# Optimization experiments

Hardware: AMD Instinct MI355X
Metric: run time of the kernel (lower is better)

The kernel has to match this reference:

```python
import jax, jax.numpy as jnp
import numpy as np

B, L, D, H = 4, 1024, 1024, 16
DH = D // H


def setup_inputs() -> dict:
    key = jax.random.key(0)
    ks = jax.random.split(key, 10)
    x_embed = jax.random.normal(ks[0], (B, L, D), dtype=jnp.float32)
    bemb = jax.random.normal(ks[1], (B, L), dtype=jnp.float32)
    s = 0.02
    Wq_w = jax.random.normal(ks[2], (D, D), dtype=jnp.float32) * s
    Wk_w = jax.random.normal(ks[3], (D, D), dtype=jnp.float32) * s
    Wv_w = jax.random.normal(ks[4], (D, D), dtype=jnp.float32) * s
    Wo_w = jax.random.normal(ks[5], (D, D), dtype=jnp.float32) * s
    Wq_b = jnp.zeros((D,), jnp.float32)
    Wk_b = jnp.zeros((D,), jnp.float32)
    Wv_b = jnp.zeros((D,), jnp.float32)
    Wo_b = jnp.zeros((D,), jnp.float32)
    return dict(x_embed=x_embed, bemb=bemb, Wq_w=Wq_w, Wq_b=Wq_b,
                Wk_w=Wk_w, Wk_b=Wk_b, Wv_w=Wv_w, Wv_b=Wv_b,
                Wo_w=Wo_w, Wo_b=Wo_b)


def reference(x_embed, bemb, Wq_w, Wq_b, Wk_w, Wk_b, Wv_w, Wv_b, Wo_w, Wo_b):
    # present[b, l] = token l of batch b participates in attention
    present = bemb > 0  # [B, L]

    def proj(w, b):
        # torch Linear: y = x W^T + b; split heads -> [B, H, L, DH]
        y = jnp.einsum('bld,ed->ble', x_embed, w) + b
        return y.reshape(B, L, H, DH).transpose(0, 2, 1, 3)

    Q = proj(Wq_w, Wq_b)
    K = proj(Wk_w, Wk_b)
    V = proj(Wv_w, Wv_b)

    scores = jnp.einsum('bhqd,bhkd->bhqk', Q, K) / jnp.sqrt(jnp.float32(DH))
    # pre-softmax column mask: absent keys -> -inf
    scores = jnp.where(present[:, None, None, :], scores, -jnp.inf)
    A = jax.nn.softmax(scores, axis=-1)  # [B, H, L, L]
    # post-softmax row mask: subtract 1 on absent query rows, then relu
    row_absent = (~present).astype(A.dtype)[:, None, :, None]  # [B,1,L,1]
    A = jnp.maximum(A - row_absent, 0.0)

    out = jnp.einsum('bhqk,bhkd->bhqd', A, V)
    out = out.transpose(0, 2, 1, 3).reshape(B, L, D)
    out = jnp.einsum('bld,ed->ble', out, Wo_w) + Wo_b
    return out, A
```

## Files before the change

### kernel.cpp

```cpp
#include <hip/hip_runtime.h>
#include <math.h>

#define BB 4
#define LL 1024
#define DD 1024
#define HH 16
#define MROWS 4096

typedef __attribute__((ext_vector_type(8))) short short8;
typedef __attribute__((ext_vector_type(4))) float f32x4;
typedef __attribute__((ext_vector_type(4))) unsigned short us4;

__device__ inline unsigned short f2bf(float f) {
    unsigned int u = __builtin_bit_cast(unsigned int, f);
    u += 0x7fffu + ((u >> 16) & 1u);
    return (unsigned short)(u >> 16);
}

__global__ __launch_bounds__(256) void cvt_bf16(const float* __restrict__ src,
                                                unsigned short* __restrict__ dst,
                                                int n4) {
    int i = blockIdx.x * 256 + threadIdx.x;
    if (i < n4) {
        float4 v = ((const float4*)src)[i];
        us4 p = { f2bf(v.x), f2bf(v.y), f2bf(v.z), f2bf(v.w) };
        ((us4*)dst)[i] = p;
    }
}

template<int OUT_MODE>
__global__ __launch_bounds__(256) void gemm128(const unsigned short* __restrict__ X,
                                               const unsigned short* __restrict__ W,
                                               const float* __restrict__ bias,
                                               void* __restrict__ Cv) {
    __shared__ unsigned short Xs[128][72];
    __shared__ unsigned short Ws[128][72];
    const int t = threadIdx.x;
    const int lane = t & 63, quad = lane >> 4, lm = lane & 15;
    const int wave = t >> 6;
    const int mo = (wave & 1) * 64, no = (wave >> 1) * 64;
    const int row0 = blockIdx.x * 128, col0 = blockIdx.y * 128;

    f32x4 acc[4][4] = {};

    for (int kc = 0; kc < 1024; kc += 64) {
        #pragma unroll
        for (int i = 0; i < 4; ++i) {
            int id = t + 256 * i; int r = id >> 3, sg = id & 7;
            *(short8*)&Xs[r][sg * 8] =
                *(const short8*)&X[(size_t)(row0 + r) * 1024 + kc + sg * 8];
            *(short8*)&Ws[r][sg * 8] =
                *(const short8*)&W[(size_t)(col0 + r) * 1024 + kc + sg * 8];
        }
        __syncthreads();
        #pragma unroll
        for (int s = 0; s < 2; ++s) {
            short8 af[4], bf[4];
            #pragma unroll
            for (int mi = 0; mi < 4; ++mi)
                af[mi] = *(const short8*)&Xs[mo + mi * 16 + lm][s * 32 + quad * 8];
            #pragma unroll
            for (int nj = 0; nj < 4; ++nj)
                bf[nj] = *(const short8*)&Ws[no + nj * 16 + lm][s * 32 + quad * 8];
            #pragma unroll
            for (int mi = 0; mi < 4; ++mi)
                #pragma unroll
                for (int nj = 0; nj < 4; ++nj)
                    acc[mi][nj] = __builtin_amdgcn_mfma_f32_16x16x32_bf16(
                        af[mi], bf[nj], acc[mi][nj], 0, 0, 0);
        }
        __syncthreads();
    }

    #pragma unroll
    for (int mi = 0; mi < 4; ++mi) {
        #pragma unroll
        for (int nj = 0; nj < 4; ++nj) {
            int gr0 = row0 + mo + mi * 16 + quad * 4;
            int gc  = col0 + no + nj * 16 + lm;
            float bv = bias[gc];
            #pragma unroll
            for (int r = 0; r < 4; ++r) {
                float val = acc[mi][nj][r] + bv;
                int gr = gr0 + r;
                if (OUT_MODE == 0) {
                    ((float*)Cv)[(size_t)gr * 1024 + gc] = val;
                } else if (OUT_MODE == 1) {
                    ((unsigned short*)Cv)[(size_t)gr * 1024 + gc] = f2bf(val);
                } else {
                    int bb = gr >> 10, l = gr & 1023;
                    int hh = gc >> 6,  dd = gc & 63;
                    ((unsigned short*)Cv)[(((size_t)bb * 16 + hh) * 64 + dd) * 1024 + l] = f2bf(val);
                }
            }
        }
    }
}

__global__ __launch_bounds__(512) void attn_fused(const unsigned short* __restrict__ Qw,
                                                  const unsigned short* __restrict__ Kw,
                                                  const unsigned short* __restrict__ Vt,
                                                  const float* __restrict__ bemb,
                                                  float* __restrict__ Aout,
                                                  unsigned short* __restrict__ attn) {
    __shared__ unsigned short Ks[128][72];
    __shared__ unsigned short Vs[64][136];
    __shared__ unsigned short Ps[8][16][132];
    __shared__ float maskadd[1024];
    const int t = threadIdx.x;
    const int lane = t & 63, quad = lane >> 4, lm = lane & 15;
    const int w = t >> 6;
    const int q0 = blockIdx.x * 128;
    const int bh = blockIdx.y;
    const int b = bh >> 4, h = bh & 15;
    const int qrow_frag = q0 + w * 16 + lm;
    const int qrow_acc0 = q0 + w * 16 + quad * 4;

    for (int i = t; i < 1024; i += 512)
        maskadd[i] = (bemb[b * 1024 + i] > 0.f) ? 0.f : -1e30f;

    short8 afq[2];
    #pragma unroll
    for (int s = 0; s < 2; ++s)
        afq[s] = *(const short8*)&Qw[(size_t)(b * 1024 + qrow_frag) * 1024 +
                                     h * 64 + s * 32 + quad * 8];

    float mrun[4], lrun[4];
    #pragma unroll
    for (int r = 0; r < 4; ++r) { mrun[r] = -INFINITY; lrun[r] = 0.f; }

    __syncthreads();

    for (int c = 0; c < 8; ++c) {
        __syncthreads();
        #pragma unroll
        for (int i = 0; i < 2; ++i) {
            int id = t + 512 * i; int r = id >> 3, sg = id & 7;
            *(short8*)&Ks[r][sg * 8] =
                *(const short8*)&Kw[(size_t)(b * 1024 + c * 128 + r) * 1024 +
                                    h * 64 + sg * 8];
        }
        __syncthreads();

        f32x4 acc[8] = {};
        #pragma unroll
        for (int s = 0; s < 2; ++s)
            #pragma unroll
            for (int nj = 0; nj < 8; ++nj) {
                short8 bfk = *(const short8*)&Ks[nj * 16 + lm][s * 32 + quad * 8];
                acc[nj] = __builtin_amdgcn_mfma_f32_16x16x32_bf16(afq[s], bfk, acc[nj], 0, 0, 0);
            }

        float cmax[4] = { -INFINITY, -INFINITY, -INFINITY, -INFINITY };
        #pragma unroll
        for (int nj = 0; nj < 8; ++nj) {
            float ma = maskadd[c * 128 + nj * 16 + lm];
            #pragma unroll
            for (int r = 0; r < 4; ++r) {
                float sv = acc[nj][r] * 0.125f + ma;
                acc[nj][r] = sv;
                cmax[r] = fmaxf(cmax[r], sv);
            }
        }
        #pragma unroll
        for (int r = 0; r < 4; ++r) {
            #pragma unroll
            for (int off = 8; off >= 1; off >>= 1)
                cmax[r] = fmaxf(cmax[r], __shfl_xor(cmax[r], off, 64));
            float mnew = fmaxf(mrun[r], cmax[r]);
            float csum = 0.f;
            #pragma unroll
            for (int nj = 0; nj < 8; ++nj)
                csum += __expf(acc[nj][r] - mnew);
            #pragma unroll
            for (int off = 8; off >= 1; off >>= 1)
                csum += __shfl_xor(csum, off, 64);
            lrun[r] = lrun[r] * __expf(mrun[r] - mnew) + csum;
            mrun[r] = mnew;
        }
    }

    float fnorm[4];
    #pragma unroll
    for (int r = 0; r < 4; ++r) {
        bool qp = bemb[b * 1024 + qrow_acc0 + r] > 0.f;
        fnorm[r] = (qp && lrun[r] > 0.f) ? (1.f / lrun[r]) : 0.f;
    }

    f32x4 oacc[4] = {};
    for (int c = 0; c < 8; ++c) {
        __syncthreads();
        #pragma unroll
        for (int i = 0; i < 2; ++i) {
            int id = t + 512 * i;
            { int r = id >> 3, sg = id & 7;
              *(short8*)&Ks[r][sg * 8] =
                  *(const short8*)&Kw[(size_t)(b * 1024 + c * 128 + r) * 1024 +
                                      h * 64 + sg * 8]; }
            { int r = id >> 4, sg = id & 15;
              *(short8*)&Vs[r][sg * 8] =
                  *(const short8*)&Vt[((size_t)bh * 64 + r) * 1024 + c * 128 + sg * 8]; }
        }
        __syncthreads();

        f32x4 acc[8] = {};
        #pragma unroll
        for (int s = 0; s < 2; ++s)
            #pragma unroll
            for (int nj = 0; nj < 8; ++nj) {
                short8 bfk = *(const short8*)&Ks[nj * 16 + lm][s * 32 + quad * 8];
                acc[nj] = __builtin_amdgcn_mfma_f32_16x16x32_bf16(afq[s], bfk, acc[nj], 0, 0, 0);
            }

        #pragma unroll
        for (int nj = 0; nj < 8; ++nj) {
            float ma = maskadd[c * 128 + nj * 16 + lm];
            #pragma unroll
            for (int r = 0; r < 4; ++r) {
                float sv = acc[nj][r] * 0.125f + ma;
                float p  = __expf(sv - mrun[r]);
                float a  = p * fnorm[r];
                Aout[((size_t)bh * 1024 + qrow_acc0 + r) * 1024 + c * 128 + nj * 16 + lm] = a;
                Ps[w][quad * 4 + r][nj * 16 + lm] = f2bf(a);
            }
        }

        #pragma unroll
        for (int ks = 0; ks < 4; ++ks) {
            short8 afp = *(const short8*)&Ps[w][lm][ks * 32 + quad * 8];
            #pragma unroll
            for (int nd = 0; nd < 4; ++nd) {
                short8 bfv = *(const short8*)&Vs[nd * 16 + lm][ks * 32 + quad * 8];
                oacc[nd] = __builtin_amdgcn_mfma_f32_16x16x32_bf16(afp, bfv, oacc[nd], 0, 0, 0);
            }
        }
    }

    #pragma unroll
    for (int nd = 0; nd < 4; ++nd)
        #pragma unroll
        for (int r = 0; r < 4; ++r)
            attn[(size_t)(b * 1024 + qrow_acc0 + r) * 1024 + h * 64 + nd * 16 + lm] =
                f2bf(oacc[nd][r]);
}

extern "C" void kernel_launch(void* const* d_in, const int* in_sizes, int n_in,
                              void* d_out, int out_size, void* d_ws, size_t ws_size,
                              hipStream_t stream) {
    const float* x    = (const float*)d_in[0];
    const float* bemb = (const float*)d_in[1];
    const float* Wq   = (const float*)d_in[2];
    const float* Wq_b = (const float*)d_in[3];
    const float* Wk   = (const float*)d_in[4];
    const float* Wk_b = (const float*)d_in[5];
    const float* Wv   = (const float*)d_in[6];
    const float* Wv_b = (const float*)d_in[7];
    const float* Wo   = (const float*)d_in[8];
    const float* Wo_b = (const float*)d_in[9];

    float* out  = (float*)d_out;
    float* Aout = out + (size_t)BB * LL * DD;

    unsigned short* x_bf  = (unsigned short*)d_ws;
    unsigned short* Wq_bf = x_bf  + (size_t)MROWS * DD;
    unsigned short* Wk_bf = Wq_bf + (size_t)DD * DD;
    unsigned short* Wv_bf = Wk_bf + (size_t)DD * DD;
    unsigned short* Wo_bf = Wv_bf + (size_t)DD * DD;
    unsigned short* Qw    = Wo_bf + (size_t)DD * DD;
    unsigned short* Kw    = Qw + (size_t)MROWS * DD;
    unsigned short* Vt    = Kw + (size_t)MROWS * DD;
    unsigned short* Aw    = x_bf;

    dim3 blk(256);
    const int n4x = MROWS * DD / 4;
    const int n4w = DD * DD / 4;
    cvt_bf16<<<dim3(n4x / 256), blk, 0, stream>>>(x,  x_bf,  n4x);
    cvt_bf16<<<dim3(n4w / 256), blk, 0, stream>>>(Wq, Wq_bf, n4w);
    cvt_bf16<<<dim3(n4w / 256), blk, 0, stream>>>(Wk, Wk_bf, n4w);
    cvt_bf16<<<dim3(n4w / 256), blk, 0, stream>>>(Wv, Wv_bf, n4w);
    cvt_bf16<<<dim3(n4w / 256), blk, 0, stream>>>(Wo, Wo_bf, n4w);

    dim3 pgrid(MROWS / 128, DD / 128);
    gemm128<1><<<pgrid, blk, 0, stream>>>(x_bf, Wq_bf, Wq_b, Qw);
    gemm128<1><<<pgrid, blk, 0, stream>>>(x_bf, Wk_bf, Wk_b, Kw);
    gemm128<2><<<pgrid, blk, 0, stream>>>(x_bf, Wv_bf, Wv_b, Vt);

    attn_fused<<<dim3(LL / 128, BB * HH), dim3(512), 0, stream>>>(
        Qw, Kw, Vt, bemb, Aout, Aw);

    gemm128<0><<<pgrid, blk, 0, stream>>>(Aw, Wo_bf, Wo_b, out);
}
```

Measured before the change: 468.5 us.

## Use direct global-to-LDS loads with XOR swizzle and merge launches

Replaces the register-staged global→LDS copies in the GEMM and attention kernels with global_load_lds 16-byte direct loads. The LDS tiles lose their padding and use an XOR swizzle to avoid bank conflicts. The five conversion kernels are merged into one launch, and the three QKV GEMMs into one launch using a z grid dimension. This is meant to cut VGPR staging, LDS bank conflicts and launch overhead. The cost is a runtime out_mode branch in the GEMM epilogue and dependence on the swizzle matching the direct-load address mapping.

```diff
diff --git a/kernel.cpp b/kernel.cpp
--- a/kernel.cpp
+++ b/kernel.cpp
@@ -17,40 +17,63 @@
     return (unsigned short)(u >> 16);
 }
 
-__global__ __launch_bounds__(256) void cvt_bf16(const float* __restrict__ src,
-                                                unsigned short* __restrict__ dst,
-                                                int n4) {
+__device__ inline void gl2lds16(const void* g, void* l) {
+    __builtin_amdgcn_global_load_lds(
+        (const __attribute__((address_space(1))) void*)g,
+        (__attribute__((address_space(3))) void*)l, 16, 0, 0);
+}
+
+__global__ __launch_bounds__(256) void cvt_all(const float* __restrict__ x,
+                                               const float* __restrict__ wq,
+                                               const float* __restrict__ wk,
+                                               const float* __restrict__ wv,
+                                               const float* __restrict__ wo,
+                                               unsigned short* __restrict__ xb,
+                                               unsigned short* __restrict__ wqb,
+                                               unsigned short* __restrict__ wkb,
+                                               unsigned short* __restrict__ wvb,
+                                               unsigned short* __restrict__ wob) {
     int i = blockIdx.x * 256 + threadIdx.x;
-    if (i < n4) {
-        float4 v = ((const float4*)src)[i];
-        us4 p = { f2bf(v.x), f2bf(v.y), f2bf(v.z), f2bf(v.w) };
-        ((us4*)dst)[i] = p;
-    }
-}
-
-template<int OUT_MODE>
-__global__ __launch_bounds__(256) void gemm128(const unsigned short* __restrict__ X,
-                                               const unsigned short* __restrict__ W,
-                                               const float* __restrict__ bias,
-                                               void* __restrict__ Cv) {
-    __shared__ unsigned short Xs[128][72];
-    __shared__ unsigned short Ws[128][72];
+    const float* src; unsigned short* dst; int k;
+    if (i < 1048576) { src = x; dst = xb; k = i; }
+    else {
+        int j = i - 1048576; int w = j >> 18; k = j & 262143;
+        src = (w == 0) ? wq : (w == 1) ? wk : (w == 2) ? wv : wo;
+        dst = (w == 0) ? wqb : (w == 1) ? wkb : (w == 2) ? wvb : wob;
+    }
+    float4 v = ((const float4*)src)[k];
+    us4 p = { f2bf(v.x), f2bf(v.y), f2bf(v.z), f2bf(v.w) };
+    ((us4*)dst)[k] = p;
+}
+
+__device__ __forceinline__ void gemm_core(const unsigned short* __restrict__ X,
+                                          const unsigned short* __restrict__ W,
+                                          const float* __restrict__ bias,
+                                          void* __restrict__ Cv, int out_mode) {
+    __shared__ unsigned short Xs[128][64];
+    __shared__ unsigned short Ws[128][64];
     const int t = threadIdx.x;
     const int lane = t & 63, quad = lane >> 4, lm = lane & 15;
     const int wave = t >> 6;
     const int mo = (wave & 1) * 64, no = (wave >> 1) * 64;
     const int row0 = blockIdx.x * 128, col0 = blockIdx.y * 128;
+    const int sw = lm & 7;
+
+    const int r_in = lane >> 3;
+    const int sg = (lane & 7) ^ r_in;
+    const int lrow = wave * 32 + r_in;
+    const unsigned short* xp = X + (size_t)(row0 + lrow) * 1024 + sg * 8;
+    const unsigned short* wp = W + (size_t)(col0 + lrow) * 1024 + sg * 8;
+    unsigned short* ldsX = &Xs[wave * 32][0];
+    unsigned short* ldsW = &Ws[wave * 32][0];
 
     f32x4 acc[4][4] = {};
 
     for (int kc = 0; kc < 1024; kc += 64) {
         #pragma unroll
-        for (int i = 0; i < 4; ++i) {
-            int id = t + 256 * i; int r = id >> 3, sg = id & 7;
-            *(short8*)&Xs[r][sg * 8] =
-                *(const short8*)&X[(size_t)(row0 + r) * 1024 + kc + sg * 8];
-            *(short8*)&Ws[r][sg * 8] =
-                *(const short8*)&W[(size_t)(col0 + r) * 1024 + kc + sg * 8];
+        for (int j = 0; j < 4; ++j) {
+            gl2lds16(xp + (size_t)j * 8192 + kc, ldsX + j * 512);
+            gl2lds16(wp + (size_t)j * 8192 + kc, ldsW + j * 512);
         }
         __syncthreads();
         #pragma unroll
@@ -58,10 +81,10 @@
             short8 af[4], bf[4];
             #pragma unroll
             for (int mi = 0; mi < 4; ++mi)
-                af[mi] = *(const short8*)&Xs[mo + mi * 16 + lm][s * 32 + quad * 8];
+                af[mi] = *(const short8*)&Xs[mo + mi * 16 + lm][((s * 4 + quad) ^ sw) * 8];
             #pragma unroll
             for (int nj = 0; nj < 4; ++nj)
-                bf[nj] = *(const short8*)&Ws[no + nj * 16 + lm][s * 32 + quad * 8];
+                bf[nj] = *(const short8*)&Ws[no + nj * 16 + lm][((s * 4 + quad) ^ sw) * 8];
             #pragma unroll
             for (int mi = 0; mi < 4; ++mi)
                 #pragma unroll
@@ -83,9 +106,9 @@
             for (int r = 0; r < 4; ++r) {
                 float val = acc[mi][nj][r] + bv;
                 int gr = gr0 + r;
-                if (OUT_MODE == 0) {
+                if (out_mode == 0) {
                     ((float*)Cv)[(size_t)gr * 1024 + gc] = val;
-                } else if (OUT_MODE == 1) {
+                } else if (out_mode == 1) {
                     ((unsigned short*)Cv)[(size_t)gr * 1024 + gc] = f2bf(val);
                 } else {
                     int bb = gr >> 10, l = gr & 1023;
@@ -97,14 +120,38 @@
     }
 }
 
+__global__ __launch_bounds__(256) void qkv_proj(const unsigned short* __restrict__ xb,
+                                                const unsigned short* __restrict__ wq,
+                                                const unsigned short* __restrict__ wk,
+                                                const unsigned short* __restrict__ wv,
+                                                const float* __restrict__ bq,
+                                                const float* __restrict__ bk,
+                                                const float* __restrict__ bv,
+                                                unsigned short* __restrict__ Qw,
+                                                unsigned short* __restrict__ Kw,
+                                                unsigned short* __restrict__ Vt) {
+    const int z = blockIdx.z;
+    const unsigned short* W = (z == 0) ? wq : (z == 1) ? wk : wv;
+    const float* b = (z == 0) ? bq : (z == 1) ? bk : bv;
+    void* C = (z == 0) ? (void*)Qw : (z == 1) ? (void*)Kw : (void*)Vt;
+    gemm_core(xb, W, b, C, (z == 2) ? 2 : 1);
+}
+
+__global__ __launch_bounds__(256) void out_proj(const unsigned short* __restrict__ Aw,
+                                                const unsigned short* __restrict__ wo,
+                                                const float* __restrict__ bo,
+                                                float* __restrict__ out) {
+    gemm_core(Aw, wo, bo, out, 0);
+}
+
 __global__ __launch_bounds__(512) void attn_fused(const unsigned short* __restrict__ Qw,
                                                   const unsigned short* __restrict__ Kw,
                                                   const unsigned short* __restrict__ Vt,
                                                   const float* __restrict__ bemb,
                                                   float* __restrict__ Aout,
                                                   unsigned short* __restrict__ attn) {
-    __shared__ unsigned short Ks[128][72];
-    __shared__ unsigned short Vs[64][136];
+    __shared__ unsigned short Ks[128][64];
+    __shared__ unsigned short Vs[64][128];
     __shared__ unsigned short Ps[8][16][132];
     __shared__ float maskadd[1024];
     const int t = threadIdx.x;
@@ -115,6 +162,16 @@
     const int b = bh >> 4, h = bh & 15;
     const int qrow_frag = q0 + w * 16 + lm;
     const int qrow_acc0 = q0 + w * 16 + quad * 4;
+    const int swk = lm & 7;
+
+    const int kr_in = lane >> 3;
+    const int ksg = (lane & 7) ^ kr_in;
+    const unsigned short* kp = Kw + (size_t)(b * 1024 + w * 16 + kr_in) * 1024 + h * 64 + ksg * 8;
+    unsigned short* ldsK = &Ks[w * 16][0];
+    const int vr_in = lane >> 4, vcg = lane & 15;
+    const int vrow = w * 8 + vr_in;
+    const unsigned short* vpbase = Vt + (size_t)bh * 64 * 1024;
+    unsigned short* ldsV = &Vs[w * 8][0];
 
     for (int i = t; i < 1024; i += 512)
         maskadd[i] = (bemb[b * 1024 + i] > 0.f) ? 0.f : -1e30f;
@@ -132,14 +189,9 @@
     __syncthreads();
 
     for (int c = 0; c < 8; ++c) {
-        __syncthreads();
-        #pragma unroll
-        for (int i = 0; i < 2; ++i) {
-            int id = t + 512 * i; int r = id >> 3, sg = id & 7;
-            *(short8*)&Ks[r][sg * 8] =
-                *(const short8*)&Kw[(size_t)(b * 1024 + c * 128 + r) * 1024 +
-                                    h * 64 + sg * 8];
-        }
+        #pragma unroll
+        for (int j = 0; j < 2; ++j)
+            gl2lds16(kp + (size_t)(c * 128 + j * 8) * 1024, ldsK + j * 512);
         __syncthreads();
 
         f32x4 acc[8] = {};
@@ -147,7 +199,7 @@
         for (int s = 0; s < 2; ++s)
             #pragma unroll
             for (int nj = 0; nj < 8; ++nj) {
-                short8 bfk = *(const short8*)&Ks[nj * 16 + lm][s * 32 + quad * 8];
+                short8 bfk = *(const short8*)&Ks[nj * 16 + lm][((s * 4 + quad) ^ swk) * 8];
                 acc[nj] = __builtin_amdgcn_mfma_f32_16x16x32_bf16(afq[s], bfk, acc[nj], 0, 0, 0);
             }
 
@@ -178,6 +230,7 @@
             lrun[r] = lrun[r] * __expf(mrun[r] - mnew) + csum;
             mrun[r] = mnew;
         }
+        __syncthreads();
     }
 
     float fnorm[4];
@@ -189,17 +242,12 @@
 
     f32x4 oacc[4] = {};
     for (int c = 0; c < 8; ++c) {
-        __syncthreads();
-        #pragma unroll
-        for (int i = 0; i < 2; ++i) {
-            int id = t + 512 * i;
-            { int r = id >> 3, sg = id & 7;
-              *(short8*)&Ks[r][sg * 8] =
-                  *(const short8*)&Kw[(size_t)(b * 1024 + c * 128 + r) * 1024 +
-                                      h * 64 + sg * 8]; }
-            { int r = id >> 4, sg = id & 15;
-              *(short8*)&Vs[r][sg * 8] =
-                  *(const short8*)&Vt[((size_t)bh * 64 + r) * 1024 + c * 128 + sg * 8]; }
+        #pragma unroll
+        for (int j = 0; j < 2; ++j) {
+            gl2lds16(kp + (size_t)(c * 128 + j * 8) * 1024, ldsK + j * 512);
+            int rl = vrow + j * 4;
+            int vsg = vcg ^ (rl & 15);
+            gl2lds16(vpbase + (size_t)rl * 1024 + c * 128 + vsg * 8, ldsV + j * 512);
         }
         __syncthreads();
 
@@ -208,7 +256,7 @@
         for (int s = 0; s < 2; ++s)
             #pragma unroll
             for (int nj = 0; nj < 8; ++nj) {
-                short8 bfk = *(const short8*)&Ks[nj * 16 + lm][s * 32 + quad * 8];
+                short8 bfk = *(const short8*)&Ks[nj * 16 + lm][((s * 4 + quad) ^ swk) * 8];
                 acc[nj] = __builtin_amdgcn_mfma_f32_16x16x32_bf16(afq[s], bfk, acc[nj], 0, 0, 0);
             }
 
@@ -230,10 +278,11 @@
             short8 afp = *(const short8*)&Ps[w][lm][ks * 32 + quad * 8];
             #pragma unroll
             for (int nd = 0; nd < 4; ++nd) {
-                short8 bfv = *(const short8*)&Vs[nd * 16 + lm][ks * 32 + quad * 8];
+                short8 bfv = *(const short8*)&Vs[nd * 16 + lm][((ks * 4 + quad) ^ lm) * 8];
                 oacc[nd] = __builtin_amdgcn_mfma_f32_16x16x32_bf16(afp, bfv, oacc[nd], 0, 0, 0);
             }
         }
+        __syncthreads();
     }
 
     #pragma unroll
@@ -271,22 +320,15 @@
     unsigned short* Vt    = Kw + (size_t)MROWS * DD;
     unsigned short* Aw    = x_bf;
 
-    dim3 blk(256);
-    const int n4x = MROWS * DD / 4;
-    const int n4w = DD * DD / 4;
-    cvt_bf16<<<dim3(n4x / 256), blk, 0, stream>>>(x,  x_bf,  n4x);
-    cvt_bf16<<<dim3(n4w / 256), blk, 0, stream>>>(Wq, Wq_bf, n4w);
-    cvt_bf16<<<dim3(n4w / 256), blk, 0, stream>>>(Wk, Wk_bf, n4w);
-    cvt_bf16<<<dim3(n4w / 256), blk, 0, stream>>>(Wv, Wv_bf, n4w);
-    cvt_bf16<<<dim3(n4w / 256), blk, 0, stream>>>(Wo, Wo_bf, n4w);
-
-    dim3 pgrid(MROWS / 128, DD / 128);
-    gemm128<1><<<pgrid, blk, 0, stream>>>(x_bf, Wq_bf, Wq_b, Qw);
-    gemm128<1><<<pgrid, blk, 0, stream>>>(x_bf, Wk_bf, Wk_b, Kw);
-    gemm128<2><<<pgrid, blk, 0, stream>>>(x_bf, Wv_bf, Wv_b, Vt);
+    cvt_all<<<dim3(8192), dim3(256), 0, stream>>>(x, Wq, Wk, Wv, Wo,
+                                                  x_bf, Wq_bf, Wk_bf, Wv_bf, Wo_bf);
+
+    qkv_proj<<<dim3(MROWS / 128, DD / 128, 3), dim3(256), 0, stream>>>(
+        x_bf, Wq_bf, Wk_bf, Wv_bf, Wq_b, Wk_b, Wv_b, Qw, Kw, Vt);
 
     attn_fused<<<dim3(LL / 128, BB * HH), dim3(512), 0, stream>>>(
         Qw, Kw, Vt, bemb, Aout, Aw);
 
-    gemm128<0><<<pgrid, blk, 0, stream>>>(Aw, Wo_bf, Wo_b, out);
-}
+    out_proj<<<dim3(MROWS / 128, DD / 128), dim3(256), 0, stream>>>(
+        Aw, Wo_bf, Wo_b, out);
+}
```

Measured after the change: 442.0 us. 1.06x faster.
